# Performance work log

Hardware: AMD Instinct MI355X
Metric: run time of the kernel (lower is better)

The kernel has to match this reference:

```python
import jax, jax.numpy as jnp
import numpy as np

WEIGHT_FACTOR = 1.0
N_CLUSTERS = 64


def setup_inputs() -> dict:
    key = jax.random.key(0)
    k1, k2, k3 = jax.random.split(key, 3)
    B, H, W = 128, 256, 256
    x = jax.random.uniform(k1, (B, H, W), dtype=jnp.float32)
    pattern_importance = jax.random.uniform(k2, (B, N_CLUSTERS), dtype=jnp.float32)
    # dense cluster map: value in [0, N_CLUSTERS) = cluster id; == N_CLUSTERS = unassigned (mask stays 1)
    cluster_id = jax.random.randint(k3, (H, W), 0, N_CLUSTERS + 1, dtype=jnp.int32)
    return {"x": x, "pattern_importance": pattern_importance, "cluster_id": cluster_id}


def reference(x, pattern_importance, cluster_id):
    # FFT2 over last two dims; torch fftshift with dim=None shifts ALL axes (incl. batch),
    # and jnp.fft.fftshift has the same default semantics.
    x_fft = jnp.fft.fftshift(jnp.fft.fft2(x))
    assigned = cluster_id < N_CLUSTERS                     # [H, W] bool
    cid = jnp.where(assigned, cluster_id, 0)               # safe gather index
    vals = pattern_importance[:, cid] * WEIGHT_FACTOR      # [B, H, W] gather-built mask values
    mask = jnp.where(assigned[None, :, :], vals, jnp.float32(1.0))
    x_reject = x_fft * mask
    x_ifft = jnp.abs(jnp.fft.ifft2(jnp.fft.ifftshift(x_reject)))
    x_diff = jnp.abs(x_ifft - x)
    x_new = jnp.stack([x, x_ifft, x_diff], axis=1)         # [B, 3, H, W]
    return (x_new, pattern_importance)
```

## Files before the change

### kernel.cpp

```cpp
#include <hip/hip_runtime.h>
#include <hip/hip_fp16.h>
#include <math.h>

#define BB 128
#define HH 256
#define WW 256
#define HW 65536
#define OUT_B_STRIDE 196608

#define LDS_FENCE() asm volatile("s_waitcnt lgkmcnt(0)" ::: "memory")

typedef float f32x4_t __attribute__((ext_vector_type(4)));

__device__ __forceinline__ void nt_store4(const float4 v, float4* p){
  f32x4_t t;
  t[0] = v.x; t[1] = v.y; t[2] = v.z; t[3] = v.w;
  __builtin_nontemporal_store(t, reinterpret_cast<f32x4_t*>(p));
}

__device__ __forceinline__ float2 cadd(float2 a, float2 b){ return make_float2(a.x+b.x, a.y+b.y); }
__device__ __forceinline__ float2 csub(float2 a, float2 b){ return make_float2(a.x-b.x, a.y-b.y); }

template<bool INV>
__device__ __forceinline__ float2 cmul_t(float2 a, float2 b){
  if (INV) return make_float2(a.x*b.x + a.y*b.y, a.y*b.x - a.x*b.y);
  return make_float2(a.x*b.x - a.y*b.y, a.x*b.y + a.y*b.x);
}

template<bool INV>
__device__ __forceinline__ void fft4(float2&a,float2&b,float2&c,float2&d){
  float2 t0 = cadd(a,c), t1 = csub(a,c);
  float2 t2 = cadd(b,d), t3 = csub(b,d);
  float2 t3r = INV ? make_float2(-t3.y, t3.x) : make_float2(t3.y, -t3.x);
  a = cadd(t0,t2);
  b = cadd(t1,t3r);
  c = csub(t0,t2);
  d = csub(t1,t3r);
}

template<bool INV>
__device__ __forceinline__ void fft16(float2 x[16]){
  #pragma unroll
  for (int j0=0;j0<4;++j0) fft4<INV>(x[j0], x[j0+4], x[j0+8], x[j0+12]);
  const float WR[10] = {1.f, 0.923879533f, 0.707106781f, 0.382683432f, 0.f,
                        0.f, -0.707106781f, 0.f, 0.f, -0.923879533f};
  const float WI[10] = {0.f, -0.382683432f, -0.707106781f, -0.923879533f, -1.f,
                        0.f, -0.707106781f, 0.f, 0.f, 0.382683432f};
  #pragma unroll
  for (int q0=1;q0<4;++q0)
    #pragma unroll
    for (int j0=1;j0<4;++j0){
      int k = j0*q0;
      x[j0+4*q0] = cmul_t<INV>(x[j0+4*q0], make_float2(WR[k], WI[k]));
    }
  #pragma unroll
  for (int q0=0;q0<4;++q0) fft4<INV>(x[4*q0], x[4*q0+1], x[4*q0+2], x[4*q0+3]);
  float2 t[16];
  #pragma unroll
  for (int q0=0;q0<4;++q0)
    #pragma unroll
    for (int q1=0;q1<4;++q1) t[q0+4*q1] = x[4*q0+q1];
  #pragma unroll
  for (int i=0;i<16;++i) x[i]=t[i];
}

__device__ __forceinline__ void build_tw_all(float2* tw, int lane){
  #pragma unroll
  for (int k=0;k<4;++k){
    int idx = lane + 64*k;
    float s,c;
    __sincosf(-6.28318530717958647692f * (float)idx / 256.0f, &s, &c);
    tw[idx] = make_float2(c, s);
  }
}

__device__ __forceinline__ uint pkh2(float2 v){
  __half2 h = __float22half2_rn(v);
  return *(uint*)&h;
}
__device__ __forceinline__ float2 uph2(uint u){
  __half2 h = *(__half2*)&u;
  return __half22float2(h);
}

union SharedU {
  float  xs[16*272];
  float2 zbuf[16*273];
  float  ybuf[16*272];
};

__global__ __launch_bounds__(256, 4) void k_row_fwd(const float* __restrict__ x,
                                                    __half2* __restrict__ S,
                                                    const int* __restrict__ cid,
                                                    unsigned char* __restrict__ cidp){
  __shared__ float2 zarena[4368];
  __shared__ float2 tw[256];
  int tid = threadIdx.x;
  int lane = tid & 63, wid = tid >> 6;
  int t = lane & 15, rl = lane >> 4;
  build_tw_all(tw, lane);

  if (blockIdx.x < 64){
    int g = (blockIdx.x*256 + tid) * 4;
    int p  = g >> 8;
    int s  = (g >> 4) & 15;
    int k1b = g & 15;
    int wfreq = 16*(p & 15) + (p >> 4);
    int w2 = (wfreq + 128) & 255;
    uchar4 v4;
    unsigned char* vp = (unsigned char*)&v4;
    #pragma unroll
    for (int i=0;i<4;++i){
      int h2 = (16*(k1b+i) + s + 128) & 255;
      int cv = cid[h2*256 + w2];
      vp[i] = (unsigned char)cv;
    }
    *(uchar4*)(cidp + g) = v4;
  }

  const float4* xb = (const float4*)x + (size_t)blockIdx.x * 2048;
  float* xsw = (float*)&zarena[wid*1092];
  #pragma unroll
  for (int j=0;j<8;++j){
    float4 v = xb[(wid*8 + j)*64 + lane];
    *(float4*)&xsw[j*272 + lane*4] = v;
  }
  LDS_FENCE();

  float2 Z[16];
  #pragma unroll
  for (int j=0;j<16;++j)
    Z[j] = make_float2(xsw[(2*rl)*272 + 16*j + t],
                       xsw[(2*rl+1)*272 + 16*j + t]);
  fft16<false>(Z);
  #pragma unroll
  for (int q=0;q<16;++q) Z[q] = cmul_t<false>(Z[q], tw[t*q]);
  float2* zb = &zarena[wid*1092 + rl*273];
  #pragma unroll
  for (int q=0;q<16;++q) zb[q*17 + t] = Z[q];
  LDS_FENCE();
  float2 Y[16];
  #pragma unroll
  for (int tt=0;tt<16;++tt) Y[tt] = zb[t*17 + tt];
  fft16<false>(Y);

  #pragma unroll
  for (int k1=0;k1<16;++k1) zb[k1*17 + t] = Y[k1];
  LDS_FENCE();
  int sel = (t == 0) ? 1 : 0;
  int tp = (16 - t) & 15;
  uint qE[16], qO[16];
  #pragma unroll
  for (int k1=0;k1<16;++k1){
    float2 M = zb[((15 - k1 + sel) & 15)*17 + tp];
    float2 Ze = make_float2(0.5f*(Y[k1].x + M.x), 0.5f*(Y[k1].y - M.y));
    float2 Zo = make_float2(0.5f*(Y[k1].y + M.y), 0.5f*(M.x - Y[k1].x));
    qE[k1] = pkh2(Ze);
    qO[k1] = pkh2(Zo);
  }

  int row0 = blockIdx.x*32 + (wid<<3) + 2*rl;
  int b = row0 >> 8, h = row0 & 255;
  uint4* dstE = (uint4*)(S + (size_t)b*HW + h*256 + t*16);
  uint4* dstO = (uint4*)(S + (size_t)b*HW + (h+1)*256 + t*16);
  #pragma unroll
  for (int k=0;k<4;++k){
    uint4 qe; qe.x = qE[4*k+0]; qe.y = qE[4*k+1]; qe.z = qE[4*k+2]; qe.w = qE[4*k+3];
    uint4 qo; qo.x = qO[4*k+0]; qo.y = qO[4*k+1]; qo.z = qO[4*k+2]; qo.w = qO[4*k+3];
    dstE[k] = qe;
    dstO[k] = qo;
  }
}

__global__ __launch_bounds__(256, 4) void k_col(__half2* __restrict__ S,
                                                const unsigned char* __restrict__ cidp,
                                                const float* __restrict__ pi){
  __shared__ SharedU sh;
  __shared__ float2 tw[256];
  __shared__ float sPI[64];
  int tid = threadIdx.x;
  int c = tid & 15, t = tid >> 4;
  int cg = blockIdx.x, b = blockIdx.y;
  build_tw_all(tw, tid & 63);
  if (tid < 64) sPI[tid] = pi[(((b + 64) & 127) << 6) + tid] * 0.25f;
  __half2* Sb = S + (size_t)b*HW;
  int p = cg*16 + c;
  float2 X[16];
  #pragma unroll
  for (int j=0;j<16;++j) X[j] = uph2(*(const uint*)&Sb[(16*j + t)*256 + p]);
  uint4 mq = *(const uint4*)(cidp + p*256 + t*16);
  __syncthreads();
  fft16<false>(X);
  #pragma unroll
  for (int q=0;q<16;++q) X[q] = cmul_t<false>(X[q], tw[t*q]);
  #pragma unroll
  for (int q=0;q<16;++q) sh.zbuf[c*273 + q*17 + t] = X[q];
  __syncthreads();
  int s = t;
  float2 Y[16];
  #pragma unroll
  for (int tt=0;tt<16;++tt) Y[tt] = sh.zbuf[c*273 + s*17 + tt];
  fft16<false>(Y);
  const uint* mw = (const uint*)&mq;
  #pragma unroll
  for (int k1=0;k1<16;++k1){
    int cv = (mw[k1>>2] >> ((k1&3)*8)) & 255;
    float m = (cv < 64) ? sPI[cv] : 0.25f;
    Y[k1].x *= m; Y[k1].y *= m;
  }
  __syncthreads();
  fft16<true>(Y);
  #pragma unroll
  for (int u=0;u<16;++u) Y[u] = cmul_t<true>(Y[u], tw[u*s]);
  #pragma unroll
  for (int u=0;u<16;++u) sh.zbuf[c*273 + u*17 + s] = Y[u];
  __syncthreads();
  float2 R[16];
  #pragma unroll
  for (int k0=0;k0<16;++k0) R[k0] = sh.zbuf[c*273 + t*17 + k0];
  fft16<true>(R);
  #pragma unroll
  for (int j=0;j<16;++j){
    *(uint*)&Sb[(16*j + t)*256 + p] = pkh2(R[j]);
  }
}

__global__ __launch_bounds__(256, 4) void k_row_inv_fused(const __half2* __restrict__ S,
                                                          const float* __restrict__ x,
                                                          const float* __restrict__ pi,
                                                          float* __restrict__ out){
  __shared__ SharedU sh;
  __shared__ float2 tw[256];
  int tid = threadIdx.x;
  int s = tid & 15, r = tid >> 4;
  int slice = blockIdx.x, b = blockIdx.y;
  build_tw_all(tw, tid & 63);
  int h = slice*16 + r;
  const uint4* src = (const uint4*)(S + (size_t)b*HW + h*256 + s*16);
  float2 X[16];
  #pragma unroll
  for (int k=0;k<4;++k){
    uint4 q = src[k];
    X[4*k+0] = uph2(q.x); X[4*k+1] = uph2(q.y);
    X[4*k+2] = uph2(q.z); X[4*k+3] = uph2(q.w);
  }
  __syncthreads();
  fft16<true>(X);
  #pragma unroll
  for (int u=0;u<16;++u) X[u] = cmul_t<true>(X[u], tw[u*s]);
  #pragma unroll
  for (int u=0;u<16;++u) sh.zbuf[r*273 + u*17 + s] = X[u];
  __syncthreads();
  float2 R[16];
  #pragma unroll
  for (int k0=0;k0<16;++k0) R[k0] = sh.zbuf[r*273 + s*17 + k0];
  fft16<true>(R);
  __syncthreads();
  const float scale = 1.0f/16384.0f;
  #pragma unroll
  for (int j=0;j<16;++j)
    sh.ybuf[r*272 + 16*j + s] = sqrtf(R[j].x*R[j].x + R[j].y*R[j].y) * scale;
  __syncthreads();
  const float4* x4 = (const float4*)x;
  float4* o4 = (float4*)out;
  size_t xbase = (size_t)b*16384 + slice*1024;
  size_t obase = (size_t)b*49152 + slice*1024;
  #pragma unroll
  for (int k=0;k<4;++k){
    int i2 = tid + k*256;
    int rr = i2 >> 6, c4 = i2 & 63;
    float4 y = *(float4*)&sh.ybuf[rr*272 + c4*4];
    float4 xv = x4[xbase + i2];
    float4 df;
    df.x = fabsf(y.x - xv.x); df.y = fabsf(y.y - xv.y);
    df.z = fabsf(y.z - xv.z); df.w = fabsf(y.w - xv.w);
    nt_store4(xv, &o4[obase + i2]);
    nt_store4(y,  &o4[obase + i2 + 16384]);
    nt_store4(df, &o4[obase + i2 + 32768]);
  }
  if (slice == 0 && b < 8){
    const float4* p4 = (const float4*)pi;
    nt_store4(p4[b*256 + tid], &o4[6291456 + b*256 + tid]);
  }
}

__global__ __launch_bounds__(256, 4) void k_row_inv_stage(const __half2* __restrict__ S,
                                                          float* __restrict__ out){
  __shared__ SharedU sh;
  __shared__ float2 tw[256];
  int tid = threadIdx.x;
  int s = tid & 15, r = tid >> 4;
  int slice = blockIdx.x, b = blockIdx.y;
  build_tw_all(tw, tid & 63);
  int h = slice*16 + r;
  const uint4* src = (const uint4*)(S + (size_t)b*HW + h*256 + s*16);
  float2 X[16];
  #pragma unroll
  for (int k=0;k<4;++k){
    uint4 q = src[k];
    X[4*k+0] = uph2(q.x); X[4*k+1] = uph2(q.y);
    X[4*k+2] = uph2(q.z); X[4*k+3] = uph2(q.w);
  }
  __syncthreads();
  fft16<true>(X);
  #pragma unroll
  for (int u=0;u<16;++u) X[u] = cmul_t<true>(X[u], tw[u*s]);
  #pragma unroll
  for (int u=0;u<16;++u) sh.zbuf[r*273 + u*17 + s] = X[u];
  __syncthreads();
  float2 R[16];
  #pragma unroll
  for (int k0=0;k0<16;++k0) R[k0] = sh.zbuf[r*273 + s*17 + k0];
  fft16<true>(R);
  const float scale = 1.0f/16384.0f;
  float* o = out + (size_t)b*OUT_B_STRIDE + h*256;
  #pragma unroll
  for (int j=0;j<16;++j)
    o[16*j + s] = sqrtf(R[j].x*R[j].x + R[j].y*R[j].y) * scale;
}

__global__ __launch_bounds__(256) void k_final(const float* __restrict__ x,
                                               const float* __restrict__ pi,
                                               float* __restrict__ out) {
  int i = blockIdx.x * 256 + threadIdx.x;
  const float4* x4 = (const float4*)x;
  float4* o4 = (float4*)out;
  int b = i >> 14;
  int r = i & 16383;
  int ch0 = b * 49152 + r;
  float4 y  = o4[ch0];
  float4 xv = x4[i];
  float4 df;
  df.x = fabsf(y.x - xv.x);
  df.y = fabsf(y.y - xv.y);
  df.z = fabsf(y.z - xv.z);
  df.w = fabsf(y.w - xv.w);
  nt_store4(xv, &o4[ch0]);
  nt_store4(y,  &o4[ch0 + 16384]);
  nt_store4(df, &o4[ch0 + 32768]);
  if (i < 2048) {
    const float4* p4 = (const float4*)pi;
    nt_store4(p4[i], &o4[6291456 + i]);
  }
}

extern "C" void kernel_launch(void* const* d_in, const int* in_sizes, int n_in,
                              void* d_out, int out_size, void* d_ws, size_t ws_size,
                              hipStream_t stream) {
  const float* x  = (const float*)d_in[0];
  const float* pi = (const float*)d_in[1];
  const int*  cid = (const int*)d_in[2];
  float* out = (float*)d_out;
  (void)in_sizes; (void)n_in; (void)out_size;

  const size_t S_bytes = (size_t)BB * HW * sizeof(__half2);
  const size_t cidp_bytes = 65536;

  if (ws_size >= S_bytes + cidp_bytes) {
    __half2* S = (__half2*)d_ws;
    unsigned char* cidp = (unsigned char*)d_ws + S_bytes;
    k_row_fwd<<<1024, 256, 0, stream>>>(x, S, cid, cidp);
    k_col<<<dim3(16, BB), 256, 0, stream>>>(S, cidp, pi);
    k_row_inv_fused<<<dim3(16, BB), 256, 0, stream>>>(S, x, pi, out);
  } else {
    __half2* S = (__half2*)out + (size_t)BB * HW;
    unsigned char* cidp = (unsigned char*)d_ws;
    k_row_fwd<<<1024, 256, 0, stream>>>(x, S, cid, cidp);
    k_col<<<dim3(16, BB), 256, 0, stream>>>(S, cidp, pi);
    k_row_inv_stage<<<dim3(16, BB), 256, 0, stream>>>(S, out);
    k_final<<<8192, 256, 0, stream>>>(x, pi, out);
  }
}
```

Before: 179.2 us.

## Fuse three FFT stages into one persistent cooperative kernel with grid syncs

Replaces the three separate launches (forward row FFT, column FFT with mask, inverse row FFT and output) with a single cooperative kernel of 512 blocks that loops over virtual blocks and separates the phases with grid-wide barriers. The goal is to remove inter-kernel launch gaps and tail effects. In exchange, occupancy is capped at 2 blocks per CU, each block runs its phase work serially, and grid syncs add their own cost. If the cooperative launch fails, it falls back to the original three launches.

```diff
diff --git a/kernel.cpp b/kernel.cpp
--- a/kernel.cpp
+++ b/kernel.cpp
@@ -1,6 +1,9 @@
 #include <hip/hip_runtime.h>
 #include <hip/hip_fp16.h>
+#include <hip/hip_cooperative_groups.h>
 #include <math.h>
+
+namespace cg = cooperative_groups;
 
 #define BB 128
 #define HH 256
@@ -89,19 +92,18 @@
   float  ybuf[16*272];
 };
 
-__global__ __launch_bounds__(256, 4) void k_row_fwd(const float* __restrict__ x,
-                                                    __half2* __restrict__ S,
-                                                    const int* __restrict__ cid,
-                                                    unsigned char* __restrict__ cidp){
-  __shared__ float2 zarena[4368];
-  __shared__ float2 tw[256];
-  int tid = threadIdx.x;
+
+__device__ __forceinline__ void phase1_rows(int vb, int tid,
+                                            const float* __restrict__ x,
+                                            __half2* __restrict__ S,
+                                            const int* __restrict__ cid,
+                                            unsigned char* __restrict__ cidp,
+                                            float2* zarena, const float2* tw){
   int lane = tid & 63, wid = tid >> 6;
   int t = lane & 15, rl = lane >> 4;
-  build_tw_all(tw, lane);
-
-  if (blockIdx.x < 64){
-    int g = (blockIdx.x*256 + tid) * 4;
+
+  if (vb < 64){
+    int g = (vb*256 + tid) * 4;
     int p  = g >> 8;
     int s  = (g >> 4) & 15;
     int k1b = g & 15;
@@ -118,7 +120,7 @@
     *(uchar4*)(cidp + g) = v4;
   }
 
-  const float4* xb = (const float4*)x + (size_t)blockIdx.x * 2048;
+  const float4* xb = (const float4*)x + (size_t)vb * 2048;
   float* xsw = (float*)&zarena[wid*1092];
   #pragma unroll
   for (int j=0;j<8;++j){
@@ -159,7 +161,7 @@
     qO[k1] = pkh2(Zo);
   }
 
-  int row0 = blockIdx.x*32 + (wid<<3) + 2*rl;
+  int row0 = vb*32 + (wid<<3) + 2*rl;
   int b = row0 >> 8, h = row0 & 255;
   uint4* dstE = (uint4*)(S + (size_t)b*HW + h*256 + t*16);
   uint4* dstO = (uint4*)(S + (size_t)b*HW + (h+1)*256 + t*16);
@@ -170,6 +172,156 @@
     dstE[k] = qe;
     dstO[k] = qo;
   }
+}
+
+__device__ __forceinline__ void phase2_cols(int vb, int tid,
+                                            __half2* __restrict__ S,
+                                            const unsigned char* __restrict__ cidp,
+                                            const float* __restrict__ pi,
+                                            SharedU* sh, const float2* tw, float* sPI){
+  int c = tid & 15, t = tid >> 4;
+  int cg_ = vb & 15, b = vb >> 4;
+  if (tid < 64) sPI[tid] = pi[(((b + 64) & 127) << 6) + tid] * 0.25f;
+  __half2* Sb = S + (size_t)b*HW;
+  int p = cg_*16 + c;
+  float2 X[16];
+  #pragma unroll
+  for (int j=0;j<16;++j) X[j] = uph2(*(const uint*)&Sb[(16*j + t)*256 + p]);
+  uint4 mq = *(const uint4*)(cidp + p*256 + t*16);
+  __syncthreads();
+  fft16<false>(X);
+  #pragma unroll
+  for (int q=0;q<16;++q) X[q] = cmul_t<false>(X[q], tw[t*q]);
+  #pragma unroll
+  for (int q=0;q<16;++q) sh->zbuf[c*273 + q*17 + t] = X[q];
+  __syncthreads();
+  int s = t;
+  float2 Y[16];
+  #pragma unroll
+  for (int tt=0;tt<16;++tt) Y[tt] = sh->zbuf[c*273 + s*17 + tt];
+  fft16<false>(Y);
+  const uint* mw = (const uint*)&mq;
+  #pragma unroll
+  for (int k1=0;k1<16;++k1){
+    int cv = (mw[k1>>2] >> ((k1&3)*8)) & 255;
+    float m = (cv < 64) ? sPI[cv] : 0.25f;
+    Y[k1].x *= m; Y[k1].y *= m;
+  }
+  __syncthreads();
+  fft16<true>(Y);
+  #pragma unroll
+  for (int u=0;u<16;++u) Y[u] = cmul_t<true>(Y[u], tw[u*s]);
+  #pragma unroll
+  for (int u=0;u<16;++u) sh->zbuf[c*273 + u*17 + s] = Y[u];
+  __syncthreads();
+  float2 R[16];
+  #pragma unroll
+  for (int k0=0;k0<16;++k0) R[k0] = sh->zbuf[c*273 + t*17 + k0];
+  fft16<true>(R);
+  #pragma unroll
+  for (int j=0;j<16;++j){
+    *(uint*)&Sb[(16*j + t)*256 + p] = pkh2(R[j]);
+  }
+}
+
+__device__ __forceinline__ void phase3_inv(int vb, int tid,
+                                           const __half2* __restrict__ S,
+                                           const float* __restrict__ x,
+                                           const float* __restrict__ pi,
+                                           float* __restrict__ out,
+                                           SharedU* sh, const float2* tw){
+  int s = tid & 15, r = tid >> 4;
+  int slice = vb & 15, b = vb >> 4;
+  int h = slice*16 + r;
+  const uint4* src = (const uint4*)(S + (size_t)b*HW + h*256 + s*16);
+  float2 X[16];
+  #pragma unroll
+  for (int k=0;k<4;++k){
+    uint4 q = src[k];
+    X[4*k+0] = uph2(q.x); X[4*k+1] = uph2(q.y);
+    X[4*k+2] = uph2(q.z); X[4*k+3] = uph2(q.w);
+  }
+  __syncthreads();
+  fft16<true>(X);
+  #pragma unroll
+  for (int u=0;u<16;++u) X[u] = cmul_t<true>(X[u], tw[u*s]);
+  #pragma unroll
+  for (int u=0;u<16;++u) sh->zbuf[r*273 + u*17 + s] = X[u];
+  __syncthreads();
+  float2 R[16];
+  #pragma unroll
+  for (int k0=0;k0<16;++k0) R[k0] = sh->zbuf[r*273 + s*17 + k0];
+  fft16<true>(R);
+  __syncthreads();
+  const float scale = 1.0f/16384.0f;
+  #pragma unroll
+  for (int j=0;j<16;++j)
+    sh->ybuf[r*272 + 16*j + s] = sqrtf(R[j].x*R[j].x + R[j].y*R[j].y) * scale;
+  __syncthreads();
+  const float4* x4 = (const float4*)x;
+  float4* o4 = (float4*)out;
+  size_t xbase = (size_t)b*16384 + slice*1024;
+  size_t obase = (size_t)b*49152 + slice*1024;
+  #pragma unroll
+  for (int k=0;k<4;++k){
+    int i2 = tid + k*256;
+    int rr = i2 >> 6, c4 = i2 & 63;
+    float4 y = *(float4*)&sh->ybuf[rr*272 + c4*4];
+    float4 xv = x4[xbase + i2];
+    float4 df;
+    df.x = fabsf(y.x - xv.x); df.y = fabsf(y.y - xv.y);
+    df.z = fabsf(y.z - xv.z); df.w = fabsf(y.w - xv.w);
+    nt_store4(xv, &o4[obase + i2]);
+    nt_store4(y,  &o4[obase + i2 + 16384]);
+    nt_store4(df, &o4[obase + i2 + 32768]);
+  }
+  if (slice == 0 && b < 8){
+    const float4* p4 = (const float4*)pi;
+    nt_store4(p4[b*256 + tid], &o4[6291456 + b*256 + tid]);
+  }
+}
+
+__global__ __launch_bounds__(256, 2) void k_fused(const float* __restrict__ x,
+                                                  __half2* __restrict__ S,
+                                                  const int* __restrict__ cid,
+                                                  unsigned char* __restrict__ cidp,
+                                                  const float* __restrict__ pi,
+                                                  float* __restrict__ out){
+  __shared__ SharedU sh;
+  __shared__ float2 tw[256];
+  __shared__ float sPI[64];
+  cg::grid_group grid = cg::this_grid();
+  int tid = threadIdx.x;
+  build_tw_all(tw, tid & 63);
+
+  #pragma unroll 1
+  for (int it=0; it<2; ++it)
+    phase1_rows(blockIdx.x*2 + it, tid, x, S, cid, cidp, (float2*)&sh, tw);
+
+  __syncthreads();
+  grid.sync();
+
+  #pragma unroll 1
+  for (int it=0; it<4; ++it)
+    phase2_cols(blockIdx.x*4 + it, tid, S, cidp, pi, &sh, tw, sPI);
+
+  grid.sync();
+
+  #pragma unroll 1
+  for (int it=0; it<4; ++it)
+    phase3_inv(blockIdx.x*4 + it, tid, S, x, pi, out, &sh, tw);
+}
+
+
+__global__ __launch_bounds__(256, 4) void k_row_fwd(const float* __restrict__ x,
+                                                    __half2* __restrict__ S,
+                                                    const int* __restrict__ cid,
+                                                    unsigned char* __restrict__ cidp){
+  __shared__ float2 zarena[4368];
+  __shared__ float2 tw[256];
+  int tid = threadIdx.x;
+  build_tw_all(tw, tid & 63);
+  phase1_rows(blockIdx.x, tid, x, S, cid, cidp, zarena, tw);
 }
 
 __global__ __launch_bounds__(256, 4) void k_col(__half2* __restrict__ S,
@@ -179,50 +331,8 @@
   __shared__ float2 tw[256];
   __shared__ float sPI[64];
   int tid = threadIdx.x;
-  int c = tid & 15, t = tid >> 4;
-  int cg = blockIdx.x, b = blockIdx.y;
   build_tw_all(tw, tid & 63);
-  if (tid < 64) sPI[tid] = pi[(((b + 64) & 127) << 6) + tid] * 0.25f;
-  __half2* Sb = S + (size_t)b*HW;
-  int p = cg*16 + c;
-  float2 X[16];
-  #pragma unroll
-  for (int j=0;j<16;++j) X[j] = uph2(*(const uint*)&Sb[(16*j + t)*256 + p]);
-  uint4 mq = *(const uint4*)(cidp + p*256 + t*16);
-  __syncthreads();
-  fft16<false>(X);
-  #pragma unroll
-  for (int q=0;q<16;++q) X[q] = cmul_t<false>(X[q], tw[t*q]);
-  #pragma unroll
-  for (int q=0;q<16;++q) sh.zbuf[c*273 + q*17 + t] = X[q];
-  __syncthreads();
-  int s = t;
-  float2 Y[16];
-  #pragma unroll
-  for (int tt=0;tt<16;++tt) Y[tt] = sh.zbuf[c*273 + s*17 + tt];
-  fft16<false>(Y);
-  const uint* mw = (const uint*)&mq;
-  #pragma unroll
-  for (int k1=0;k1<16;++k1){
-    int cv = (mw[k1>>2] >> ((k1&3)*8)) & 255;
-    float m = (cv < 64) ? sPI[cv] : 0.25f;
-    Y[k1].x *= m; Y[k1].y *= m;
-  }
-  __syncthreads();
-  fft16<true>(Y);
-  #pragma unroll
-  for (int u=0;u<16;++u) Y[u] = cmul_t<true>(Y[u], tw[u*s]);
-  #pragma unroll
-  for (int u=0;u<16;++u) sh.zbuf[c*273 + u*17 + s] = Y[u];
-  __syncthreads();
-  float2 R[16];
-  #pragma unroll
-  for (int k0=0;k0<16;++k0) R[k0] = sh.zbuf[c*273 + t*17 + k0];
-  fft16<true>(R);
-  #pragma unroll
-  for (int j=0;j<16;++j){
-    *(uint*)&Sb[(16*j + t)*256 + p] = pkh2(R[j]);
-  }
+  phase2_cols(blockIdx.y*16 + blockIdx.x, tid, S, cidp, pi, &sh, tw, sPI);
 }
 
 __global__ __launch_bounds__(256, 4) void k_row_inv_fused(const __half2* __restrict__ S,
@@ -232,56 +342,8 @@
   __shared__ SharedU sh;
   __shared__ float2 tw[256];
   int tid = threadIdx.x;
-  int s = tid & 15, r = tid >> 4;
-  int slice = blockIdx.x, b = blockIdx.y;
   build_tw_all(tw, tid & 63);
-  int h = slice*16 + r;
-  const uint4* src = (const uint4*)(S + (size_t)b*HW + h*256 + s*16);
-  float2 X[16];
-  #pragma unroll
-  for (int k=0;k<4;++k){
-    uint4 q = src[k];
-    X[4*k+0] = uph2(q.x); X[4*k+1] = uph2(q.y);
-    X[4*k+2] = uph2(q.z); X[4*k+3] = uph2(q.w);
-  }
-  __syncthreads();
-  fft16<true>(X);
-  #pragma unroll
-  for (int u=0;u<16;++u) X[u] = cmul_t<true>(X[u], tw[u*s]);
-  #pragma unroll
-  for (int u=0;u<16;++u) sh.zbuf[r*273 + u*17 + s] = X[u];
-  __syncthreads();
-  float2 R[16];
-  #pragma unroll
-  for (int k0=0;k0<16;++k0) R[k0] = sh.zbuf[r*273 + s*17 + k0];
-  fft16<true>(R);
-  __syncthreads();
-  const float scale = 1.0f/16384.0f;
-  #pragma unroll
-  for (int j=0;j<16;++j)
-    sh.ybuf[r*272 + 16*j + s] = sqrtf(R[j].x*R[j].x + R[j].y*R[j].y) * scale;
-  __syncthreads();
-  const float4* x4 = (const float4*)x;
-  float4* o4 = (float4*)out;
-  size_t xbase = (size_t)b*16384 + slice*1024;
-  size_t obase = (size_t)b*49152 + slice*1024;
-  #pragma unroll
-  for (int k=0;k<4;++k){
-    int i2 = tid + k*256;
-    int rr = i2 >> 6, c4 = i2 & 63;
-    float4 y = *(float4*)&sh.ybuf[rr*272 + c4*4];
-    float4 xv = x4[xbase + i2];
-    float4 df;
-    df.x = fabsf(y.x - xv.x); df.y = fabsf(y.y - xv.y);
-    df.z = fabsf(y.z - xv.z); df.w = fabsf(y.w - xv.w);
-    nt_store4(xv, &o4[obase + i2]);
-    nt_store4(y,  &o4[obase + i2 + 16384]);
-    nt_store4(df, &o4[obase + i2 + 32768]);
-  }
-  if (slice == 0 && b < 8){
-    const float4* p4 = (const float4*)pi;
-    nt_store4(p4[b*256 + tid], &o4[6291456 + b*256 + tid]);
-  }
+  phase3_inv(blockIdx.y*16 + blockIdx.x, tid, S, x, pi, out, &sh, tw);
 }
 
 __global__ __launch_bounds__(256, 4) void k_row_inv_stage(const __half2* __restrict__ S,
@@ -359,9 +421,17 @@
   if (ws_size >= S_bytes + cidp_bytes) {
     __half2* S = (__half2*)d_ws;
     unsigned char* cidp = (unsigned char*)d_ws + S_bytes;
-    k_row_fwd<<<1024, 256, 0, stream>>>(x, S, cid, cidp);
-    k_col<<<dim3(16, BB), 256, 0, stream>>>(S, cidp, pi);
-    k_row_inv_fused<<<dim3(16, BB), 256, 0, stream>>>(S, x, pi, out);
+
+    void* ka[6];
+    ka[0] = (void*)&x;  ka[1] = (void*)&S;   ka[2] = (void*)&cid;
+    ka[3] = (void*)&cidp; ka[4] = (void*)&pi; ka[5] = (void*)&out;
+    hipError_t err = hipLaunchCooperativeKernel((const void*)k_fused,
+                                                dim3(512), dim3(256), ka, 0, stream);
+    if (err != hipSuccess) {
+      k_row_fwd<<<1024, 256, 0, stream>>>(x, S, cid, cidp);
+      k_col<<<dim3(16, BB), 256, 0, stream>>>(S, cidp, pi);
+      k_row_inv_fused<<<dim3(16, BB), 256, 0, stream>>>(S, x, pi, out);
+    }
   } else {
     __half2* S = (__half2*)out + (size_t)BB * HW;
     unsigned char* cidp = (unsigned char*)d_ws;
```

Measured after the change: 332.1 us. +85.3%, slower.
